# Kernel tuning notes

Hardware: AMD Instinct MI355X
Metric: run time of the kernel (lower is better)

Reference implementation:

```python
import jax, jax.numpy as jnp
import numpy as np

# Module config (matches init_kwargs); num_heads must be 1 for the original
# torch code to type-check (score_proj: Linear(d_model, num_heads) applied to
# a head_dim-sized last axis, then squeeze(-1)).
B, S, D, H = 4, 512, 256, 1
DH = D // H  # head_dim == d_model when H == 1


def _linear_init(k, out_f, in_f):
    bound = 1.0 / np.sqrt(in_f)
    kw, kb = jax.random.split(k)
    W = jax.random.uniform(kw, (out_f, in_f), jnp.float32, -bound, bound)
    b = jax.random.uniform(kb, (out_f,), jnp.float32, -bound, bound)
    return W, b


def setup_inputs() -> dict:
    key = jax.random.key(0)
    ks = jax.random.split(key, 8)
    Wq, bq = _linear_init(ks[3], D, D)
    Wk, bk = _linear_init(ks[4], D, D)
    Wv, bv = _linear_init(ks[5], D, D)
    Ws, bs = _linear_init(ks[6], H, D)   # score_proj: d_model -> num_heads
    Wo, bo = _linear_init(ks[7], D, D)
    return {
        "query": jax.random.normal(ks[0], (B, S, D), jnp.float32),
        "key": jax.random.normal(ks[1], (B, S, D), jnp.float32),
        "value": jax.random.normal(ks[2], (B, S, D), jnp.float32),
        "Wq": Wq, "bq": bq, "Wk": Wk, "bk": bk, "Wv": Wv, "bv": bv,
        "Ws": Ws, "bs": bs, "Wo": Wo, "bo": bo,
    }


def reference(query, key, value, Wq, bq, Wk, bk, Wv, bv, Ws, bs, Wo, bo):
    b, s, _ = query.shape
    # Projections, split into heads: (B, H, S, DH)
    q = (query @ Wq.T + bq).reshape(b, s, H, DH).transpose(0, 2, 1, 3)
    k = (key @ Wk.T + bk).reshape(b, s, H, DH).transpose(0, 2, 1, 3)
    v = (value @ Wv.T + bv).reshape(b, s, H, DH).transpose(0, 2, 1, 3)
    # Bahdanau additive scores: tanh of pairwise sum -> (B, H, Sq, Sk, DH)
    t = jnp.tanh(q[:, :, :, None, :] + k[:, :, None, :, :])
    # score_proj (out_features == 1 when H == 1), then squeeze(-1)
    scores = jnp.einsum('bhqkd,od->bhqko', t, Ws) + bs  # (B,H,Sq,Sk,1)
    scores = scores[..., 0]                              # (B,H,Sq,Sk)
    attn = jax.nn.softmax(scores, axis=-1)
    # Weighted sum of values, merge heads back: (B, S, D)
    attended = jnp.einsum('bhqk,bhkd->bqhd', attn, v).reshape(b, s, D)
    out = attended @ Wo.T + bo  # dropout p=0.0 (eval) -> identity
    return out, attn
```

## Files before the change

kernel.cpp:

```cpp
#include <hip/hip_runtime.h>

typedef __attribute__((ext_vector_type(8))) short short8;
typedef __attribute__((ext_vector_type(4))) float f32x4;

constexpr int BATCH = 4;
constexpr int SEQ   = 512;
constexpr int DM    = 256;

#define MFMA(a,b,c) __builtin_amdgcn_mfma_f32_16x16x32_bf16((a),(b),(c),0,0,0)

__device__ __forceinline__ unsigned short bf16h(float x) {
    unsigned u = __float_as_uint(x);
    return (unsigned short)((u + 0x7FFF + ((u >> 16) & 1)) >> 16);
}
__device__ __forceinline__ float bf16f(unsigned short h) {
    return __uint_as_float(((unsigned)h) << 16);
}
__device__ __forceinline__ float exp2x_clamped(float x) {
    x = fminf(5.0f, fmaxf(-5.0f, x));
    return __builtin_amdgcn_exp2f(x * 2.8853900817779268f);
}
__device__ __forceinline__ void cvt8(const float* s, int4& h, int4& l) {
    unsigned hw[8], lw[8];
    #pragma unroll
    for (int j = 0; j < 8; ++j) {
        unsigned short hb = bf16h(s[j]);
        hw[j] = hb;
        lw[j] = bf16h(s[j] - bf16f(hb));
    }
    h.x = (int)(hw[0] | (hw[1] << 16)); h.y = (int)(hw[2] | (hw[3] << 16));
    h.z = (int)(hw[4] | (hw[5] << 16)); h.w = (int)(hw[6] | (hw[7] << 16));
    l.x = (int)(lw[0] | (lw[1] << 16)); l.y = (int)(lw[2] | (lw[3] << 16));
    l.z = (int)(lw[4] | (lw[5] << 16)); l.w = (int)(lw[6] | (lw[7] << 16));
}

__global__ __launch_bounds__(256) void conv_w(
    const float* __restrict__ Wq, const float* __restrict__ Wk,
    const float* __restrict__ Wv, const float* __restrict__ Wo,
    ushort* Wqh, ushort* Wql, ushort* Wkh, ushort* Wkl,
    ushort* Wvh, ushort* Wvl, ushort* Woh, ushort* Wol)
{
    const float* s; ushort* h; ushort* l;
    switch (blockIdx.y) {
        case 0: s = Wq; h = Wqh; l = Wql; break;
        case 1: s = Wk; h = Wkh; l = Wkl; break;
        case 2: s = Wv; h = Wvh; l = Wvl; break;
        default:s = Wo; h = Woh; l = Wol; break;
    }
    int idx = (blockIdx.x * 256 + threadIdx.x) * 8;
    float4 f0 = *(const float4*)(s + idx);
    float4 f1 = *(const float4*)(s + idx + 4);
    float xs[8] = {f0.x, f0.y, f0.z, f0.w, f1.x, f1.y, f1.z, f1.w};
    int4 ph, pl;
    cvt8(xs, ph, pl);
    *(int4*)&h[idx] = ph;
    *(int4*)&l[idx] = pl;
}

template<int EPI, int ASRC>
__device__ __forceinline__ void mfma_core(
    const ushort* __restrict__ Ah, const ushort* __restrict__ Al,
    const float*  __restrict__ A0, const float*  __restrict__ A1, long ldA,
    const ushort* __restrict__ Bh, const ushort* __restrict__ Bl, long ldB,
    float* __restrict__ C, long ldC, const float* __restrict__ bias,
    ushort* __restrict__ Th, ushort* __restrict__ Tl, long ldT)
{
    __shared__ short lds[16384];
    const int tid = threadIdx.x;
    const int i0 = tid, i1 = tid + 256;
    const int r0 = ((i0 >> 7) << 4) | (i0 & 15), r1 = ((i1 >> 7) << 4) | (i1 & 15);
    const int c0 = ((i0 >> 4) & 7) * 8,          c1 = ((i1 >> 4) & 7) * 8;
    const long a0o = (long)r0 * ldA + c0, a1o = (long)r1 * ldA + c1;
    const long b0o = (long)r0 * ldB + c0, b1o = (long)r1 * ldB + c1;

    int4 rah0, rah1, ral0, ral1, rbh0, rbh1, rbl0, rbl1;
    float4 fa00, fa01, fa10, fa11, fb00, fb01, fb10, fb11;

    auto issue_loads = [&](int it) {
        long off = (long)it * 64;
        if constexpr (ASRC != 0) {
            fa00 = *(const float4*)(A0 + a0o + off); fa01 = *(const float4*)(A0 + a0o + off + 4);
            fa10 = *(const float4*)(A0 + a1o + off); fa11 = *(const float4*)(A0 + a1o + off + 4);
            if constexpr (ASRC == 2) {
                fb00 = *(const float4*)(A1 + a0o + off); fb01 = *(const float4*)(A1 + a0o + off + 4);
                fb10 = *(const float4*)(A1 + a1o + off); fb11 = *(const float4*)(A1 + a1o + off + 4);
            }
        } else {
            rah0 = *(const int4*)(Ah + a0o + off); rah1 = *(const int4*)(Ah + a1o + off);
            ral0 = *(const int4*)(Al + a0o + off); ral1 = *(const int4*)(Al + a1o + off);
        }
        rbh0 = *(const int4*)(Bh + b0o + off); rbh1 = *(const int4*)(Bh + b1o + off);
        rbl0 = *(const int4*)(Bl + b0o + off); rbl1 = *(const int4*)(Bl + b1o + off);
    };
    auto write_lds = [&]() {
        if constexpr (ASRC != 0) {
            float s0[8], s1[8];
            if constexpr (ASRC == 2) {
                s0[0]=fa00.x+fb00.x; s0[1]=fa00.y+fb00.y; s0[2]=fa00.z+fb00.z; s0[3]=fa00.w+fb00.w;
                s0[4]=fa01.x+fb01.x; s0[5]=fa01.y+fb01.y; s0[6]=fa01.z+fb01.z; s0[7]=fa01.w+fb01.w;
                s1[0]=fa10.x+fb10.x; s1[1]=fa10.y+fb10.y; s1[2]=fa10.z+fb10.z; s1[3]=fa10.w+fb10.w;
                s1[4]=fa11.x+fb11.x; s1[5]=fa11.y+fb11.y; s1[6]=fa11.z+fb11.z; s1[7]=fa11.w+fb11.w;
            } else {
                s0[0]=fa00.x; s0[1]=fa00.y; s0[2]=fa00.z; s0[3]=fa00.w;
                s0[4]=fa01.x; s0[5]=fa01.y; s0[6]=fa01.z; s0[7]=fa01.w;
                s1[0]=fa10.x; s1[1]=fa10.y; s1[2]=fa10.z; s1[3]=fa10.w;
                s1[4]=fa11.x; s1[5]=fa11.y; s1[6]=fa11.z; s1[7]=fa11.w;
            }
            int4 h, l2;
            cvt8(s0, h, l2);
            *(int4*)&lds[i0 * 8] = h; *(int4*)&lds[4096 + i0 * 8] = l2;
            cvt8(s1, h, l2);
            *(int4*)&lds[i1 * 8] = h; *(int4*)&lds[4096 + i1 * 8] = l2;
        } else {
            *(int4*)&lds[i0 * 8] = rah0;        *(int4*)&lds[i1 * 8] = rah1;
            *(int4*)&lds[4096 + i0 * 8] = ral0; *(int4*)&lds[4096 + i1 * 8] = ral1;
        }
        *(int4*)&lds[8192  + i0 * 8] = rbh0; *(int4*)&lds[8192  + i1 * 8] = rbh1;
        *(int4*)&lds[12288 + i0 * 8] = rbl0; *(int4*)&lds[12288 + i1 * 8] = rbl1;
    };

    const int l = tid & 63, w = tid >> 6;
    const int ms = (w >> 1) * 2, ns = (w & 1) * 2;
    f32x4 acc00 = {0,0,0,0}, acc01 = {0,0,0,0}, acc10 = {0,0,0,0}, acc11 = {0,0,0,0};

    issue_loads(0);
    for (int it = 0; it < 4; ++it) {
        write_lds();
        __syncthreads();
        if (it < 3) issue_loads(it + 1);
        const int lo = l * 8;
        #pragma unroll
        for (int ks = 0; ks < 2; ++ks) {
            short8 a0h = *(const short8*)&lds[((ms    ) * 2 + ks) * 512 + lo];
            short8 a1h = *(const short8*)&lds[((ms + 1) * 2 + ks) * 512 + lo];
            short8 a0l = *(const short8*)&lds[4096 + ((ms    ) * 2 + ks) * 512 + lo];
            short8 a1l = *(const short8*)&lds[4096 + ((ms + 1) * 2 + ks) * 512 + lo];
            short8 b0h = *(const short8*)&lds[8192 + ((ns    ) * 2 + ks) * 512 + lo];
            short8 b1h = *(const short8*)&lds[8192 + ((ns + 1) * 2 + ks) * 512 + lo];
            short8 b0l = *(const short8*)&lds[12288 + ((ns    ) * 2 + ks) * 512 + lo];
            short8 b1l = *(const short8*)&lds[12288 + ((ns + 1) * 2 + ks) * 512 + lo];
            acc00 = MFMA(a0h, b0h, acc00); acc00 = MFMA(a0h, b0l, acc00); acc00 = MFMA(a0l, b0h, acc00);
            acc01 = MFMA(a0h, b1h, acc01); acc01 = MFMA(a0h, b1l, acc01); acc01 = MFMA(a0l, b1h, acc01);
            acc10 = MFMA(a1h, b0h, acc10); acc10 = MFMA(a1h, b0l, acc10); acc10 = MFMA(a1l, b0h, acc10);
            acc11 = MFMA(a1h, b1h, acc11); acc11 = MFMA(a1h, b1l, acc11); acc11 = MFMA(a1l, b1h, acc11);
        }
        __syncthreads();
    }

    auto epi = [&](int i, int j, f32x4 a) {
        const int n  = (ns + j) * 16 + (l & 15);
        const int mb = (ms + i) * 16 + (l >> 4) * 4;
        if constexpr (EPI == 1) {
            float bb = bias[n];
            float x0 = a.x + bb, x1 = a.y + bb, x2 = a.z + bb, x3 = a.w + bb;
            unsigned short h0 = bf16h(x0), h1 = bf16h(x1), h2 = bf16h(x2), h3 = bf16h(x3);
            int2 ph, pl;
            ph.x = (int)(h0 | ((unsigned)h1 << 16));
            ph.y = (int)(h2 | ((unsigned)h3 << 16));
            pl.x = (int)(bf16h(x0 - bf16f(h0)) | ((unsigned)bf16h(x1 - bf16f(h1)) << 16));
            pl.y = (int)(bf16h(x2 - bf16f(h2)) | ((unsigned)bf16h(x3 - bf16f(h3)) << 16));
            *(int2*)&Th[(long)n * ldT + mb] = ph;
            *(int2*)&Tl[(long)n * ldT + mb] = pl;
        } else {
            float bb = (EPI == 2) ? 0.f : bias[n];
            float xs[4] = {a.x, a.y, a.z, a.w};
            #pragma unroll
            for (int r = 0; r < 4; ++r) {
                float x = xs[r] + bb;
                if constexpr (EPI == 0) x = exp2x_clamped(x);
                C[(long)(mb + r) * ldC + n] = x;
            }
        }
    };
    epi(0, 0, acc00); epi(0, 1, acc01); epi(1, 0, acc10); epi(1, 1, acc11);
}

__global__ __launch_bounds__(256) void proj_mfma(
    const float* __restrict__ q, const float* __restrict__ k, const float* __restrict__ v,
    const ushort* Wqh, const ushort* Wql, const ushort* Wkh, const ushort* Wkl,
    const ushort* Wvh, const ushort* Wvl,
    const float* bq, const float* bk, const float* bv,
    float* Eq, float* Ek, ushort* vpTh, ushort* vpTl)
{
    const int z = blockIdx.z;
    const long m0 = blockIdx.x * 64, n0 = blockIdx.y * 64;
    const float* A; const ushort *Bh, *Bl; const float* bias;
    if (z == 0)      { A = q; Bh = Wqh; Bl = Wql; bias = bq; }
    else if (z == 1) { A = k; Bh = Wkh; Bl = Wkl; bias = bk; }
    else             { A = v; Bh = Wvh; Bl = Wvl; bias = bv; }
    A += m0 * 256; Bh += n0 * 256; Bl += n0 * 256; bias += n0;
    if (z < 2) {
        float* C = (z ? Ek : Eq) + m0 * 256 + n0;
        mfma_core<0, 1>(nullptr, nullptr, A, nullptr, 256, Bh, Bl, 256,
                        C, 256, bias, nullptr, nullptr, 0);
    } else {
        mfma_core<1, 1>(nullptr, nullptr, A, nullptr, 256, Bh, Bl, 256,
                        nullptr, 0, bias,
                        vpTh + n0 * 2048 + m0, vpTl + n0 * 2048 + m0, 2048);
    }
}

__global__ __launch_bounds__(256) void attnv_mfma(
    const ushort* attn_h, const ushort* attn_l,
    const ushort* vpTh, const ushort* vpTl, float* att0, float* att1)
{
    const int z = blockIdx.z, b = z >> 1, h = z & 1;
    const long m0 = blockIdx.x * 64, n0 = blockIdx.y * 64;
    const long arow = (long)b * SEQ + m0;
    const ushort* Ah = attn_h + arow * SEQ + h * 256;
    const ushort* Al = attn_l + arow * SEQ + h * 256;
    const ushort* Bh = vpTh + n0 * 2048 + (long)b * SEQ + h * 256;
    const ushort* Bl = vpTl + n0 * 2048 + (long)b * SEQ + h * 256;
    float* C = (h ? att1 : att0) + arow * DM + n0;
    mfma_core<2, 0>(Ah, Al, nullptr, nullptr, SEQ, Bh, Bl, 2048,
                    C, DM, nullptr, nullptr, nullptr, 0);
}

__global__ __launch_bounds__(256) void out_mfma(
    const float* att0, const float* att1,
    const ushort* Woh, const ushort* Wol, const float* bo, float* out)
{
    const long m0 = blockIdx.x * 64, n0 = blockIdx.y * 64;
    mfma_core<3, 2>(nullptr, nullptr, att0 + m0 * 256, att1 + m0 * 256, 256,
                    Woh + n0 * 256, Wol + n0 * 256, 256,
                    out + m0 * 256 + n0, 256, bo + n0, nullptr, nullptr, 0);
}

__global__ __launch_bounds__(256) void scores_kernel(
    const float* __restrict__ Eq, const float* __restrict__ Ek,
    const float* __restrict__ Ws, float* __restrict__ part)
{
    __shared__ __align__(16) float qL[64][68];
    __shared__ __align__(16) float kL[64][68];
    const int z = blockIdx.z;
    const int b = z >> 2, c = z & 3;
    const int c0 = c * 64;
    const int q0 = blockIdx.x * 64, k0 = blockIdx.y * 64;
    const int tid = threadIdx.x;
    const int qi = tid >> 4, ki = tid & 15;
    const float* Eqb = Eq + ((long)b * SEQ + q0) * DM + c0;
    const float* Ekb = Ek + ((long)b * SEQ + k0) * DM + c0;

    #pragma unroll
    for (int i = 0; i < 4; ++i) {
        int f = i * 256 + tid;
        int r = f >> 4, col = (f & 15) << 2;
        *(float4*)&qL[r][col] = *(const float4*)(Eqb + (long)r * DM + col);
        *(float4*)&kL[r][col] = *(const float4*)(Ekb + (long)r * DM + col);
    }
    __syncthreads();

    float acc[4][4] = {};
    #pragma unroll 2
    for (int d = 0; d < 64; d += 4) {
        float4 w4 = *(const float4*)(Ws + c0 + d);
        float4 av[4], bv[4];
        #pragma unroll
        for (int i = 0; i < 4; ++i) av[i] = *(const float4*)&qL[qi + 16 * i][d];
        #pragma unroll
        for (int j = 0; j < 4; ++j) bv[j] = *(const float4*)&kL[ki + 16 * j][d];
        #pragma unroll
        for (int i = 0; i < 4; ++i)
            #pragma unroll
            for (int j = 0; j < 4; ++j) {
                float xp = fmaf(av[i].x, bv[j].x, 1.0f);
                float yp = fmaf(av[i].y, bv[j].y, 1.0f);
                float zp = fmaf(av[i].z, bv[j].z, 1.0f);
                float wp = fmaf(av[i].w, bv[j].w, 1.0f);
                float xy = xp * yp, zw = zp * wp;
                float n1 = fmaf(w4.x, yp, w4.y * xp);
                float n2 = fmaf(w4.z, wp, w4.w * zp);
                float num = fmaf(n1, zw, n2 * xy);
                acc[i][j] = fmaf(num, __builtin_amdgcn_rcpf(xy * zw), acc[i][j]);
            }
    }

    float* pb = part + (long)c * (BATCH * SEQ * SEQ) + (long)b * SEQ * SEQ;
    #pragma unroll
    for (int i = 0; i < 4; ++i) {
        float* row = pb + (long)(q0 + qi + 16 * i) * SEQ + k0 + ki;
        #pragma unroll
        for (int j = 0; j < 4; ++j) row[16 * j] = acc[i][j];
    }
}

__global__ __launch_bounds__(256) void softmax_kernel(
    const float* __restrict__ part, float* __restrict__ attn,
    ushort* __restrict__ attn_h, ushort* __restrict__ attn_l)
{
    __shared__ float red[8];
    const int tid = threadIdx.x;
    const long row = blockIdx.x;
    constexpr long PS = (long)BATCH * SEQ * SEQ;
    const float* p = part + row * SEQ + tid * 2;
    float2 v0 = *(const float2*)(p);
    float2 v1 = *(const float2*)(p + PS);
    float2 v2 = *(const float2*)(p + 2 * PS);
    float2 v3 = *(const float2*)(p + 3 * PS);
    float sx = -2.0f * ((v0.x + v1.x) + (v2.x + v3.x));
    float sy = -2.0f * ((v0.y + v1.y) + (v2.y + v3.y));

    float m = fmaxf(sx, sy);
    #pragma unroll
    for (int off = 32; off; off >>= 1) m = fmaxf(m, __shfl_xor(m, off));
    int wave = tid >> 6;
    if ((tid & 63) == 0) red[wave] = m;
    __syncthreads();
    m = fmaxf(fmaxf(red[0], red[1]), fmaxf(red[2], red[3]));
    constexpr float L2E = 1.4426950408889634f;
    float e0 = __builtin_amdgcn_exp2f((sx - m) * L2E);
    float e1 = __builtin_amdgcn_exp2f((sy - m) * L2E);
    float s = e0 + e1;
    #pragma unroll
    for (int off = 32; off; off >>= 1) s += __shfl_xor(s, off);
    if ((tid & 63) == 0) red[4 + wave] = s;
    __syncthreads();
    float tot = (red[4] + red[5]) + (red[6] + red[7]);
    float inv = __builtin_amdgcn_rcpf(tot);
    float2 o; o.x = e0 * inv; o.y = e1 * inv;
    *(float2*)(attn + row * SEQ + tid * 2) = o;

    unsigned short h0 = bf16h(o.x), h1 = bf16h(o.y);
    unsigned hp = h0 | ((unsigned)h1 << 16);
    unsigned lp = bf16h(o.x - bf16f(h0)) | ((unsigned)bf16h(o.y - bf16f(h1)) << 16);
    *(unsigned*)&attn_h[row * SEQ + tid * 2] = hp;
    *(unsigned*)&attn_l[row * SEQ + tid * 2] = lp;
}

extern "C" void kernel_launch(void* const* d_in, const int* in_sizes, int n_in,
                              void* d_out, int out_size, void* d_ws, size_t ws_size,
                              hipStream_t stream) {
    const float* query = (const float*)d_in[0];
    const float* key   = (const float*)d_in[1];
    const float* value = (const float*)d_in[2];
    const float* Wq = (const float*)d_in[3];
    const float* bq = (const float*)d_in[4];
    const float* Wk = (const float*)d_in[5];
    const float* bk = (const float*)d_in[6];
    const float* Wv = (const float*)d_in[7];
    const float* bv = (const float*)d_in[8];
    const float* Ws = (const float*)d_in[9];
    const float* Wo = (const float*)d_in[11];
    const float* bo = (const float*)d_in[12];

    float* out  = (float*)d_out;
    float* attn = (float*)d_out + (long)BATCH * SEQ * DM;

    float* ws = (float*)d_ws;
    float* Eq   = ws;
    float* Ek   = ws + 524288;
    float* part = ws + 1048576;
    float* att0 = part;
    float* att1 = part + 524288;
    ushort* u = (ushort*)(ws + 1048576 + 4194304);
    ushort* Wqh = u;              ushort* Wql = Wqh + 65536;
    ushort* Wkh = Wql + 65536;    ushort* Wkl = Wkh + 65536;
    ushort* Wvh = Wkl + 65536;    ushort* Wvl = Wvh + 65536;
    ushort* Woh = Wvl + 65536;    ushort* Wol = Woh + 65536;
    ushort* vpTh   = Wol + 65536;    ushort* vpTl   = vpTh + 524288;
    ushort* attn_h = vpTl + 524288;  ushort* attn_l = attn_h + 1048576;

    conv_w       <<<dim3(32, 4),    256, 0, stream>>>(Wq, Wk, Wv, Wo,
                                                      Wqh, Wql, Wkh, Wkl,
                                                      Wvh, Wvl, Woh, Wol);
    proj_mfma    <<<dim3(32, 4, 3), 256, 0, stream>>>(query, key, value,
                                                      Wqh, Wql, Wkh, Wkl, Wvh, Wvl,
                                                      bq, bk, bv, Eq, Ek, vpTh, vpTl);
    scores_kernel<<<dim3(8, 8, 16), 256, 0, stream>>>(Eq, Ek, Ws, part);
    softmax_kernel<<<dim3(2048),    256, 0, stream>>>(part, attn, attn_h, attn_l);
    attnv_mfma   <<<dim3(8, 4, 8),  256, 0, stream>>>(attn_h, attn_l, vpTh, vpTl, att0, att1);
    out_mfma     <<<dim3(32, 4),    256, 0, stream>>>(att0, att1, Woh, Wol, bo, out);
}
```

Before: 72.38 us.

## Fuse weight bf16 split into GEMMs, double-buffer LDS, halve score partials

Drops the separate conv_w kernel. Weights are now loaded as fp32 and split into hi/lo bf16 inside the MFMA GEMM loader. The GEMM core gains a double-buffered LDS ping-pong, which removes one barrier per k-step and overlaps the LDS write with compute. The scores kernel now loops over two 64-wide channel chunks per block instead of four separate partial planes, so it writes half as many partial planes and softmax reads two instead of four. The trade-off is redundant weight conversion per block, double the LDS use, and fewer score blocks in flight.

```diff
diff --git a/kernel.cpp b/kernel.cpp
--- a/kernel.cpp
+++ b/kernel.cpp
@@ -34,38 +34,16 @@
     l.z = (int)(lw[4] | (lw[5] << 16)); l.w = (int)(lw[6] | (lw[7] << 16));
 }
 
-__global__ __launch_bounds__(256) void conv_w(
-    const float* __restrict__ Wq, const float* __restrict__ Wk,
-    const float* __restrict__ Wv, const float* __restrict__ Wo,
-    ushort* Wqh, ushort* Wql, ushort* Wkh, ushort* Wkl,
-    ushort* Wvh, ushort* Wvl, ushort* Woh, ushort* Wol)
-{
-    const float* s; ushort* h; ushort* l;
-    switch (blockIdx.y) {
-        case 0: s = Wq; h = Wqh; l = Wql; break;
-        case 1: s = Wk; h = Wkh; l = Wkl; break;
-        case 2: s = Wv; h = Wvh; l = Wvl; break;
-        default:s = Wo; h = Woh; l = Wol; break;
-    }
-    int idx = (blockIdx.x * 256 + threadIdx.x) * 8;
-    float4 f0 = *(const float4*)(s + idx);
-    float4 f1 = *(const float4*)(s + idx + 4);
-    float xs[8] = {f0.x, f0.y, f0.z, f0.w, f1.x, f1.y, f1.z, f1.w};
-    int4 ph, pl;
-    cvt8(xs, ph, pl);
-    *(int4*)&h[idx] = ph;
-    *(int4*)&l[idx] = pl;
-}
-
-template<int EPI, int ASRC>
+template<int EPI, int ASRC, int BSRC>
 __device__ __forceinline__ void mfma_core(
     const ushort* __restrict__ Ah, const ushort* __restrict__ Al,
     const float*  __restrict__ A0, const float*  __restrict__ A1, long ldA,
-    const ushort* __restrict__ Bh, const ushort* __restrict__ Bl, long ldB,
+    const ushort* __restrict__ Bh, const ushort* __restrict__ Bl,
+    const float*  __restrict__ B0, long ldB,
     float* __restrict__ C, long ldC, const float* __restrict__ bias,
     ushort* __restrict__ Th, ushort* __restrict__ Tl, long ldT)
 {
-    __shared__ short lds[16384];
+    __shared__ short lds[32768];
     const int tid = threadIdx.x;
     const int i0 = tid, i1 = tid + 256;
     const int r0 = ((i0 >> 7) << 4) | (i0 & 15), r1 = ((i1 >> 7) << 4) | (i1 & 15);
@@ -74,7 +52,8 @@
     const long b0o = (long)r0 * ldB + c0, b1o = (long)r1 * ldB + c1;
 
     int4 rah0, rah1, ral0, ral1, rbh0, rbh1, rbl0, rbl1;
-    float4 fa00, fa01, fa10, fa11, fb00, fb01, fb10, fb11;
+    float4 fa00, fa01, fa10, fa11, ga00, ga01, ga10, ga11;
+    float4 gb00, gb01, gb10, gb11;
 
     auto issue_loads = [&](int it) {
         long off = (long)it * 64;
@@ -82,24 +61,30 @@
             fa00 = *(const float4*)(A0 + a0o + off); fa01 = *(const float4*)(A0 + a0o + off + 4);
             fa10 = *(const float4*)(A0 + a1o + off); fa11 = *(const float4*)(A0 + a1o + off + 4);
             if constexpr (ASRC == 2) {
-                fb00 = *(const float4*)(A1 + a0o + off); fb01 = *(const float4*)(A1 + a0o + off + 4);
-                fb10 = *(const float4*)(A1 + a1o + off); fb11 = *(const float4*)(A1 + a1o + off + 4);
+                ga00 = *(const float4*)(A1 + a0o + off); ga01 = *(const float4*)(A1 + a0o + off + 4);
+                ga10 = *(const float4*)(A1 + a1o + off); ga11 = *(const float4*)(A1 + a1o + off + 4);
             }
         } else {
             rah0 = *(const int4*)(Ah + a0o + off); rah1 = *(const int4*)(Ah + a1o + off);
             ral0 = *(const int4*)(Al + a0o + off); ral1 = *(const int4*)(Al + a1o + off);
         }
-        rbh0 = *(const int4*)(Bh + b0o + off); rbh1 = *(const int4*)(Bh + b1o + off);
-        rbl0 = *(const int4*)(Bl + b0o + off); rbl1 = *(const int4*)(Bl + b1o + off);
+        if constexpr (BSRC == 1) {
+            gb00 = *(const float4*)(B0 + b0o + off); gb01 = *(const float4*)(B0 + b0o + off + 4);
+            gb10 = *(const float4*)(B0 + b1o + off); gb11 = *(const float4*)(B0 + b1o + off + 4);
+        } else {
+            rbh0 = *(const int4*)(Bh + b0o + off); rbh1 = *(const int4*)(Bh + b1o + off);
+            rbl0 = *(const int4*)(Bl + b0o + off); rbl1 = *(const int4*)(Bl + b1o + off);
+        }
     };
-    auto write_lds = [&]() {
+    auto write_lds = [&](int buf) {
+        const int bo = buf * 16384;
         if constexpr (ASRC != 0) {
             float s0[8], s1[8];
             if constexpr (ASRC == 2) {
-                s0[0]=fa00.x+fb00.x; s0[1]=fa00.y+fb00.y; s0[2]=fa00.z+fb00.z; s0[3]=fa00.w+fb00.w;
-                s0[4]=fa01.x+fb01.x; s0[5]=fa01.y+fb01.y; s0[6]=fa01.z+fb01.z; s0[7]=fa01.w+fb01.w;
-                s1[0]=fa10.x+fb10.x; s1[1]=fa10.y+fb10.y; s1[2]=fa10.z+fb10.z; s1[3]=fa10.w+fb10.w;
-                s1[4]=fa11.x+fb11.x; s1[5]=fa11.y+fb11.y; s1[6]=fa11.z+fb11.z; s1[7]=fa11.w+fb11.w;
+                s0[0]=fa00.x+ga00.x; s0[1]=fa00.y+ga00.y; s0[2]=fa00.z+ga00.z; s0[3]=fa00.w+ga00.w;
+                s0[4]=fa01.x+ga01.x; s0[5]=fa01.y+ga01.y; s0[6]=fa01.z+ga01.z; s0[7]=fa01.w+ga01.w;
+                s1[0]=fa10.x+ga10.x; s1[1]=fa10.y+ga10.y; s1[2]=fa10.z+ga10.z; s1[3]=fa10.w+ga10.w;
+                s1[4]=fa11.x+ga11.x; s1[5]=fa11.y+ga11.y; s1[6]=fa11.z+ga11.z; s1[7]=fa11.w+ga11.w;
             } else {
                 s0[0]=fa00.x; s0[1]=fa00.y; s0[2]=fa00.z; s0[3]=fa00.w;
                 s0[4]=fa01.x; s0[5]=fa01.y; s0[6]=fa01.z; s0[7]=fa01.w;
@@ -108,15 +93,25 @@
             }
             int4 h, l2;
             cvt8(s0, h, l2);
-            *(int4*)&lds[i0 * 8] = h; *(int4*)&lds[4096 + i0 * 8] = l2;
+            *(int4*)&lds[bo + i0 * 8] = h; *(int4*)&lds[bo + 4096 + i0 * 8] = l2;
             cvt8(s1, h, l2);
-            *(int4*)&lds[i1 * 8] = h; *(int4*)&lds[4096 + i1 * 8] = l2;
-        } else {
-            *(int4*)&lds[i0 * 8] = rah0;        *(int4*)&lds[i1 * 8] = rah1;
-            *(int4*)&lds[4096 + i0 * 8] = ral0; *(int4*)&lds[4096 + i1 * 8] = ral1;
-        }
-        *(int4*)&lds[8192  + i0 * 8] = rbh0; *(int4*)&lds[8192  + i1 * 8] = rbh1;
-        *(int4*)&lds[12288 + i0 * 8] = rbl0; *(int4*)&lds[12288 + i1 * 8] = rbl1;
+            *(int4*)&lds[bo + i1 * 8] = h; *(int4*)&lds[bo + 4096 + i1 * 8] = l2;
+        } else {
+            *(int4*)&lds[bo + i0 * 8] = rah0;        *(int4*)&lds[bo + i1 * 8] = rah1;
+            *(int4*)&lds[bo + 4096 + i0 * 8] = ral0; *(int4*)&lds[bo + 4096 + i1 * 8] = ral1;
+        }
+        if constexpr (BSRC == 1) {
+            float s0[8] = {gb00.x, gb00.y, gb00.z, gb00.w, gb01.x, gb01.y, gb01.z, gb01.w};
+            float s1[8] = {gb10.x, gb10.y, gb10.z, gb10.w, gb11.x, gb11.y, gb11.z, gb11.w};
+            int4 h, l2;
+            cvt8(s0, h, l2);
+            *(int4*)&lds[bo + 8192 + i0 * 8] = h; *(int4*)&lds[bo + 12288 + i0 * 8] = l2;
+            cvt8(s1, h, l2);
+            *(int4*)&lds[bo + 8192 + i1 * 8] = h; *(int4*)&lds[bo + 12288 + i1 * 8] = l2;
+        } else {
+            *(int4*)&lds[bo + 8192  + i0 * 8] = rbh0; *(int4*)&lds[bo + 8192  + i1 * 8] = rbh1;
+            *(int4*)&lds[bo + 12288 + i0 * 8] = rbl0; *(int4*)&lds[bo + 12288 + i1 * 8] = rbl1;
+        }
     };
 
     const int l = tid & 63, w = tid >> 6;
@@ -124,27 +119,31 @@
     f32x4 acc00 = {0,0,0,0}, acc01 = {0,0,0,0}, acc10 = {0,0,0,0}, acc11 = {0,0,0,0};
 
     issue_loads(0);
+    write_lds(0);
+    __syncthreads();
     for (int it = 0; it < 4; ++it) {
-        write_lds();
-        __syncthreads();
         if (it < 3) issue_loads(it + 1);
+        const int bo = (it & 1) * 16384;
         const int lo = l * 8;
         #pragma unroll
         for (int ks = 0; ks < 2; ++ks) {
-            short8 a0h = *(const short8*)&lds[((ms    ) * 2 + ks) * 512 + lo];
-            short8 a1h = *(const short8*)&lds[((ms + 1) * 2 + ks) * 512 + lo];
-            short8 a0l = *(const short8*)&lds[4096 + ((ms    ) * 2 + ks) * 512 + lo];
-            short8 a1l = *(const short8*)&lds[4096 + ((ms + 1) * 2 + ks) * 512 + lo];
-            short8 b0h = *(const short8*)&lds[8192 + ((ns    ) * 2 + ks) * 512 + lo];
-            short8 b1h = *(const short8*)&lds[8192 + ((ns + 1) * 2 + ks) * 512 + lo];
-            short8 b0l = *(const short8*)&lds[12288 + ((ns    ) * 2 + ks) * 512 + lo];
-            short8 b1l = *(const short8*)&lds[12288 + ((ns + 1) * 2 + ks) * 512 + lo];
+            short8 a0h = *(const short8*)&lds[bo + ((ms    ) * 2 + ks) * 512 + lo];
+            short8 a1h = *(const short8*)&lds[bo + ((ms + 1) * 2 + ks) * 512 + lo];
+            short8 a0l = *(const short8*)&lds[bo + 4096 + ((ms    ) * 2 + ks) * 512 + lo];
+            short8 a1l = *(const short8*)&lds[bo + 4096 + ((ms + 1) * 2 + ks) * 512 + lo];
+            short8 b0h = *(const short8*)&lds[bo + 8192 + ((ns    ) * 2 + ks) * 512 + lo];
+            short8 b1h = *(const short8*)&lds[bo + 8192 + ((ns + 1) * 2 + ks) * 512 + lo];
+            short8 b0l = *(const short8*)&lds[bo + 12288 + ((ns    ) * 2 + ks) * 512 + lo];
+            short8 b1l = *(const short8*)&lds[bo + 12288 + ((ns + 1) * 2 + ks) * 512 + lo];
             acc00 = MFMA(a0h, b0h, acc00); acc00 = MFMA(a0h, b0l, acc00); acc00 = MFMA(a0l, b0h, acc00);
             acc01 = MFMA(a0h, b1h, acc01); acc01 = MFMA(a0h, b1l, acc01); acc01 = MFMA(a0l, b1h, acc01);
             acc10 = MFMA(a1h, b0h, acc10); acc10 = MFMA(a1h, b0l, acc10); acc10 = MFMA(a1l, b0h, acc10);
             acc11 = MFMA(a1h, b1h, acc11); acc11 = MFMA(a1h, b1l, acc11); acc11 = MFMA(a1l, b1h, acc11);
         }
-        __syncthreads();
+        if (it < 3) {
+            write_lds((it + 1) & 1);
+            __syncthreads();
+        }
     }
 
     auto epi = [&](int i, int j, f32x4 a) {
@@ -177,26 +176,27 @@
 
 __global__ __launch_bounds__(256) void proj_mfma(
     const float* __restrict__ q, const float* __restrict__ k, const float* __restrict__ v,
-    const ushort* Wqh, const ushort* Wql, const ushort* Wkh, const ushort* Wkl,
-    const ushort* Wvh, const ushort* Wvl,
+    const float* __restrict__ Wq, const float* __restrict__ Wk, const float* __restrict__ Wv,
     const float* bq, const float* bk, const float* bv,
     float* Eq, float* Ek, ushort* vpTh, ushort* vpTl)
 {
     const int z = blockIdx.z;
     const long m0 = blockIdx.x * 64, n0 = blockIdx.y * 64;
-    const float* A; const ushort *Bh, *Bl; const float* bias;
-    if (z == 0)      { A = q; Bh = Wqh; Bl = Wql; bias = bq; }
-    else if (z == 1) { A = k; Bh = Wkh; Bl = Wkl; bias = bk; }
-    else             { A = v; Bh = Wvh; Bl = Wvl; bias = bv; }
-    A += m0 * 256; Bh += n0 * 256; Bl += n0 * 256; bias += n0;
+    const float* A; const float* B; const float* bias;
+    if (z == 0)      { A = q; B = Wq; bias = bq; }
+    else if (z == 1) { A = k; B = Wk; bias = bk; }
+    else             { A = v; B = Wv; bias = bv; }
+    A += m0 * 256; B += n0 * 256; bias += n0;
     if (z < 2) {
         float* C = (z ? Ek : Eq) + m0 * 256 + n0;
-        mfma_core<0, 1>(nullptr, nullptr, A, nullptr, 256, Bh, Bl, 256,
-                        C, 256, bias, nullptr, nullptr, 0);
+        mfma_core<0, 1, 1>(nullptr, nullptr, A, nullptr, 256,
+                           nullptr, nullptr, B, 256,
+                           C, 256, bias, nullptr, nullptr, 0);
     } else {
-        mfma_core<1, 1>(nullptr, nullptr, A, nullptr, 256, Bh, Bl, 256,
-                        nullptr, 0, bias,
-                        vpTh + n0 * 2048 + m0, vpTl + n0 * 2048 + m0, 2048);
+        mfma_core<1, 1, 1>(nullptr, nullptr, A, nullptr, 256,
+                           nullptr, nullptr, B, 256,
+                           nullptr, 0, bias,
+                           vpTh + n0 * 2048 + m0, vpTl + n0 * 2048 + m0, 2048);
     }
 }
 
@@ -212,18 +212,19 @@
     const ushort* Bh = vpTh + n0 * 2048 + (long)b * SEQ + h * 256;
     const ushort* Bl = vpTl + n0 * 2048 + (long)b * SEQ + h * 256;
     float* C = (h ? att1 : att0) + arow * DM + n0;
-    mfma_core<2, 0>(Ah, Al, nullptr, nullptr, SEQ, Bh, Bl, 2048,
-                    C, DM, nullptr, nullptr, nullptr, 0);
+    mfma_core<2, 0, 0>(Ah, Al, nullptr, nullptr, SEQ,
+                       Bh, Bl, nullptr, 2048,
+                       C, DM, nullptr, nullptr, nullptr, 0);
 }
 
 __global__ __launch_bounds__(256) void out_mfma(
     const float* att0, const float* att1,
-    const ushort* Woh, const ushort* Wol, const float* bo, float* out)
+    const float* Wo, const float* bo, float* out)
 {
     const long m0 = blockIdx.x * 64, n0 = blockIdx.y * 64;
-    mfma_core<3, 2>(nullptr, nullptr, att0 + m0 * 256, att1 + m0 * 256, 256,
-                    Woh + n0 * 256, Wol + n0 * 256, 256,
-                    out + m0 * 256 + n0, 256, bo + n0, nullptr, nullptr, 0);
+    mfma_core<3, 2, 1>(nullptr, nullptr, att0 + m0 * 256, att1 + m0 * 256, 256,
+                       nullptr, nullptr, Wo + n0 * 256, 256,
+                       out + m0 * 256 + n0, 256, bo + n0, nullptr, nullptr, 0);
 }
 
 __global__ __launch_bounds__(256) void scores_kernel(
@@ -233,46 +234,48 @@
     __shared__ __align__(16) float qL[64][68];
     __shared__ __align__(16) float kL[64][68];
     const int z = blockIdx.z;
-    const int b = z >> 2, c = z & 3;
-    const int c0 = c * 64;
+    const int b = z >> 1, c = z & 1;
     const int q0 = blockIdx.x * 64, k0 = blockIdx.y * 64;
     const int tid = threadIdx.x;
     const int qi = tid >> 4, ki = tid & 15;
-    const float* Eqb = Eq + ((long)b * SEQ + q0) * DM + c0;
-    const float* Ekb = Ek + ((long)b * SEQ + k0) * DM + c0;
-
-    #pragma unroll
-    for (int i = 0; i < 4; ++i) {
-        int f = i * 256 + tid;
-        int r = f >> 4, col = (f & 15) << 2;
-        *(float4*)&qL[r][col] = *(const float4*)(Eqb + (long)r * DM + col);
-        *(float4*)&kL[r][col] = *(const float4*)(Ekb + (long)r * DM + col);
-    }
-    __syncthreads();
 
     float acc[4][4] = {};
-    #pragma unroll 2
-    for (int d = 0; d < 64; d += 4) {
-        float4 w4 = *(const float4*)(Ws + c0 + d);
-        float4 av[4], bv[4];
+    for (int cc = 0; cc < 2; ++cc) {
+        const int c0 = c * 128 + cc * 64;
+        const float* Eqb = Eq + ((long)b * SEQ + q0) * DM + c0;
+        const float* Ekb = Ek + ((long)b * SEQ + k0) * DM + c0;
+        if (cc) __syncthreads();
         #pragma unroll
-        for (int i = 0; i < 4; ++i) av[i] = *(const float4*)&qL[qi + 16 * i][d];
-        #pragma unroll
-        for (int j = 0; j < 4; ++j) bv[j] = *(const float4*)&kL[ki + 16 * j][d];
-        #pragma unroll
-        for (int i = 0; i < 4; ++i)
+        for (int i = 0; i < 4; ++i) {
+            int f = i * 256 + tid;
+            int r = f >> 4, col = (f & 15) << 2;
+            *(float4*)&qL[r][col] = *(const float4*)(Eqb + (long)r * DM + col);
+            *(float4*)&kL[r][col] = *(const float4*)(Ekb + (long)r * DM + col);
+        }
+        __syncthreads();
+        #pragma unroll 2
+        for (int d = 0; d < 64; d += 4) {
+            float4 w4 = *(const float4*)(Ws + c0 + d);
+            float4 av[4], bv[4];
             #pragma unroll
-            for (int j = 0; j < 4; ++j) {
-                float xp = fmaf(av[i].x, bv[j].x, 1.0f);
-                float yp = fmaf(av[i].y, bv[j].y, 1.0f);
-                float zp = fmaf(av[i].z, bv[j].z, 1.0f);
-                float wp = fmaf(av[i].w, bv[j].w, 1.0f);
-                float xy = xp * yp, zw = zp * wp;
-                float n1 = fmaf(w4.x, yp, w4.y * xp);
-                float n2 = fmaf(w4.z, wp, w4.w * zp);
-                float num = fmaf(n1, zw, n2 * xy);
-                acc[i][j] = fmaf(num, __builtin_amdgcn_rcpf(xy * zw), acc[i][j]);
-            }
+            for (int i = 0; i < 4; ++i) av[i] = *(const float4*)&qL[qi + 16 * i][d];
+            #pragma unroll
+            for (int j = 0; j < 4; ++j) bv[j] = *(const float4*)&kL[ki + 16 * j][d];
+            #pragma unroll
+            for (int i = 0; i < 4; ++i)
+                #pragma unroll
+                for (int j = 0; j < 4; ++j) {
+                    float xp = fmaf(av[i].x, bv[j].x, 1.0f);
+                    float yp = fmaf(av[i].y, bv[j].y, 1.0f);
+                    float zp = fmaf(av[i].z, bv[j].z, 1.0f);
+                    float wp = fmaf(av[i].w, bv[j].w, 1.0f);
+                    float xy = xp * yp, zw = zp * wp;
+                    float n1 = fmaf(w4.x, yp, w4.y * xp);
+                    float n2 = fmaf(w4.z, wp, w4.w * zp);
+                    float num = fmaf(n1, zw, n2 * xy);
+                    acc[i][j] = fmaf(num, __builtin_amdgcn_rcpf(xy * zw), acc[i][j]);
+                }
+        }
     }
 
     float* pb = part + (long)c * (BATCH * SEQ * SEQ) + (long)b * SEQ * SEQ;
@@ -295,10 +298,8 @@
     const float* p = part + row * SEQ + tid * 2;
     float2 v0 = *(const float2*)(p);
     float2 v1 = *(const float2*)(p + PS);
-    float2 v2 = *(const float2*)(p + 2 * PS);
-    float2 v3 = *(const float2*)(p + 3 * PS);
-    float sx = -2.0f * ((v0.x + v1.x) + (v2.x + v3.x));
-    float sy = -2.0f * ((v0.y + v1.y) + (v2.y + v3.y));
+    float sx = -2.0f * (v0.x + v1.x);
+    float sy = -2.0f * (v0.y + v1.y);
 
     float m = fmaxf(sx, sy);
     #pragma unroll
@@ -352,22 +353,15 @@
     float* part = ws + 1048576;
     float* att0 = part;
     float* att1 = part + 524288;
-    ushort* u = (ushort*)(ws + 1048576 + 4194304);
-    ushort* Wqh = u;              ushort* Wql = Wqh + 65536;
-    ushort* Wkh = Wql + 65536;    ushort* Wkl = Wkh + 65536;
-    ushort* Wvh = Wkl + 65536;    ushort* Wvl = Wvh + 65536;
-    ushort* Woh = Wvl + 65536;    ushort* Wol = Woh + 65536;
-    ushort* vpTh   = Wol + 65536;    ushort* vpTl   = vpTh + 524288;
+    ushort* u = (ushort*)(ws + 1048576 + 2097152);
+    ushort* vpTh   = u;              ushort* vpTl   = vpTh + 524288;
     ushort* attn_h = vpTl + 524288;  ushort* attn_l = attn_h + 1048576;
 
-    conv_w       <<<dim3(32, 4),    256, 0, stream>>>(Wq, Wk, Wv, Wo,
-                                                      Wqh, Wql, Wkh, Wkl,
-                                                      Wvh, Wvl, Woh, Wol);
     proj_mfma    <<<dim3(32, 4, 3), 256, 0, stream>>>(query, key, value,
-                                                      Wqh, Wql, Wkh, Wkl, Wvh, Wvl,
-                                                      bq, bk, bv, Eq, Ek, vpTh, vpTl);
-    scores_kernel<<<dim3(8, 8, 16), 256, 0, stream>>>(Eq, Ek, Ws, part);
+                                                      Wq, Wk, Wv, bq, bk, bv,
+                                                      Eq, Ek, vpTh, vpTl);
+    scores_kernel<<<dim3(8, 8, 8),  256, 0, stream>>>(Eq, Ek, Ws, part);
     softmax_kernel<<<dim3(2048),    256, 0, stream>>>(part, attn, attn_h, attn_l);
     attnv_mfma   <<<dim3(8, 4, 8),  256, 0, stream>>>(attn_h, attn_l, vpTh, vpTl, att0, att1);
-    out_mfma     <<<dim3(32, 4),    256, 0, stream>>>(att0, att1, Woh, Wol, bo, out);
-}
+    out_mfma     <<<dim3(32, 4),    256, 0, stream>>>(att0, att1, Wo, bo, out);
+}
```

Result: slower. 74.93 us (+3.5%).
